# Performance work log

Measured on AMD Instinct MI355X. Metric: run time of the kernel, lower is better.

The kernel has to match this reference:

```python
import jax, jax.numpy as jnp
import numpy as np

B, N, C = 16, 4096, 64          # batch, input points, feature channels
NPOINT, NSAMPLE = 1024, 32      # FPS centroids, neighbors per group
MLP = [64, 64, 128]


def setup_inputs() -> dict:
    key = jax.random.key(0)
    ks = jax.random.split(key, 8)
    xyz = jax.random.uniform(ks[0], (B, N, 3), jnp.float32)
    points = jax.random.normal(ks[1], (B, N, C), jnp.float32)
    inp = {"xyz": xyz, "points": points}
    dims = [3 + C] + MLP  # use_xyz=True -> concat local coords
    for i in range(3):
        inp[f"w{i}"] = jax.random.normal(ks[2 + i], (dims[i], dims[i + 1]), jnp.float32) * (1.0 / np.sqrt(dims[i]))
        inp[f"b{i}"] = jnp.zeros((dims[i + 1],), jnp.float32)
    return inp


def _fps(pts, npoint):
    # iterative farthest point sampling for one cloud (N,3) -> (npoint,) int32
    n = pts.shape[0]
    def step(carry, _):
        dists, last = carry
        d = jnp.sum((pts - pts[last]) ** 2, axis=-1)
        dists = jnp.minimum(dists, d)
        return (dists, jnp.argmax(dists).astype(jnp.int32)), last
    _, idx = jax.lax.scan(step, (jnp.full((n,), 1e10, pts.dtype), jnp.int32(0)), None, length=npoint)
    return idx


def _knn(new_xyz, xyz, k):
    # squared distances (B,S,N) -> k nearest indices (B,S,k)
    d = (jnp.sum(new_xyz ** 2, -1)[..., None]
         - 2.0 * jnp.einsum('bsd,bnd->bsn', new_xyz, xyz)
         + jnp.sum(xyz ** 2, -1)[:, None, :])
    _, idx = jax.lax.top_k(-d, k)
    return idx


def reference(xyz, points, w0, b0, w1, b1, w2, b2):
    bidx = jnp.arange(B)[:, None, None]
    fps_idx = jax.vmap(lambda p: _fps(p, NPOINT))(xyz)            # (B,S)
    new_xyz = jnp.take_along_axis(xyz, fps_idx[..., None], axis=1)  # (B,S,3)
    idx = _knn(new_xyz, xyz, NSAMPLE)                             # (B,S,K)
    grouped_xyz = xyz[bidx, idx] - new_xyz[:, :, None, :]         # local coords (B,S,K,3)
    grouped_pts = points[bidx, idx]                               # (B,S,K,C)
    new_points = jnp.concatenate([grouped_xyz, grouped_pts], axis=-1)
    for w, bias in ((w0, b0), (w1, b1), (w2, b2)):                # 1x1 conv2d MLP
        new_points = jax.nn.relu(jnp.einsum('bskc,cf->bskf', new_points, w) + bias)
    new_points = jnp.max(new_points, axis=2)                      # max over neighbors
    return new_xyz, new_points
```

## Files before the change

kernel.cpp:

```cpp
#include <hip/hip_runtime.h>

#define NB 16
#define NPTS 4096
#define NC 64
#define NS 1024
#define NK 32

typedef float v2f __attribute__((ext_vector_type(2)));
typedef short bf16x8 __attribute__((ext_vector_type(8)));
typedef float f32x4 __attribute__((ext_vector_type(4)));

#define DPP_ROR_I(x, N) __builtin_amdgcn_update_dpp(0, (int)(x), 0x120 + (N), 0xf, 0xf, false)
#define MFMA16(a, b, c) __builtin_amdgcn_mfma_f32_16x16x32_bf16((a), (b), (c), 0, 0, 0)

static __device__ __forceinline__ float max3f(float a, float b, float c) {
    return fmaxf(fmaxf(a, b), c);
}
static __device__ __forceinline__ unsigned min3u(unsigned a, unsigned b, unsigned c) {
    const unsigned m = a < b ? a : b;
    return m < c ? m : c;
}
static __device__ __forceinline__ unsigned short f2bf(float f) {
    const unsigned u = __float_as_uint(f);
    const unsigned r = 0x7FFFu + ((u >> 16) & 1u);
    return (unsigned short)((u + r) >> 16);
}
static __device__ __forceinline__ float bf2f(unsigned short h) {
    return __uint_as_float(((unsigned)h) << 16);
}
static __device__ __forceinline__ unsigned pkhi(float a, float b) {
    return (unsigned)f2bf(a) | ((unsigned)f2bf(b) << 16);
}
static __device__ __forceinline__ unsigned pklo(float a, float b) {
    const float la = a - bf2f(f2bf(a));
    const float lb = b - bf2f(f2bf(b));
    return (unsigned)f2bf(la) | ((unsigned)f2bf(lb) << 16);
}

__global__ __launch_bounds__(256) void fps_kernel(const float* __restrict__ xyz,
                                                  float* __restrict__ out_xyz) {
    __shared__ float4 pts4[NPTS];
    __shared__ float hx[NS], hy[NS], hz[NS];
    __shared__ unsigned wk[2][4][2];

    const int b = blockIdx.x;
    const int t = threadIdx.x;
    const int wv = t >> 6;
    const int lane = t & 63;

    const float* xb = xyz + (size_t)b * NPTS * 3;
    for (int i = t; i < NPTS; i += 256) {
        pts4[i] = make_float4(xb[3 * i], xb[3 * i + 1], xb[3 * i + 2], 0.0f);
    }
    __syncthreads();

    v2f PX[8], PY[8], PZ[8];
    float dm[16];
#pragma unroll
    for (int k = 0; k < 8; ++k) {
        const float4 p0 = pts4[t + (2 * k) * 256];
        const float4 p1 = pts4[t + (2 * k + 1) * 256];
        PX[k].x = p0.x; PX[k].y = p1.x;
        PY[k].x = p0.y; PY[k].y = p1.y;
        PZ[k].x = p0.z; PZ[k].y = p1.z;
        dm[2 * k] = 1e10f; dm[2 * k + 1] = 1e10f;
    }

    const float4 c0 = pts4[0];
    float cx = c0.x, cy = c0.y, cz = c0.z;

    for (int s = 0; s < NS; ++s) {
        if (t == 0) { hx[s] = cx; hy[s] = cy; hz[s] = cz; }

        const v2f cX = { cx, cx };
        const v2f cY = { cy, cy };
        const v2f cZ = { cz, cz };
#pragma unroll
        for (int k = 0; k < 8; ++k) {
            const v2f dX = PX[k] - cX;
            const v2f dY = PY[k] - cY;
            const v2f dZ = PZ[k] - cZ;
            const v2f t1 = dX * dX;
            const v2f t2 = dY * dY;
            const v2f t3 = dZ * dZ;
            const v2f ss = (t1 + t2) + t3;
            dm[2 * k] = fminf(dm[2 * k], ss.x);
            dm[2 * k + 1] = fminf(dm[2 * k + 1], ss.y);
        }

        const float ta = max3f(dm[0], dm[1], dm[2]);
        const float tb = max3f(dm[3], dm[4], dm[5]);
        const float tc = max3f(dm[6], dm[7], dm[8]);
        const float td = max3f(dm[9], dm[10], dm[11]);
        const float te = max3f(dm[12], dm[13], dm[14]);
        const float mv = fmaxf(max3f(ta, tb, tc), max3f(td, te, dm[15]));

        unsigned u[16];
#pragma unroll
        for (int j = 0; j < 16; ++j)
            u[j] = (dm[j] == mv) ? (unsigned)(t + j * 256) : 0xFFFFFFFFu;
        const unsigned ua = min3u(u[0], u[1], u[2]);
        const unsigned ub = min3u(u[3], u[4], u[5]);
        const unsigned uc = min3u(u[6], u[7], u[8]);
        const unsigned ud = min3u(u[9], u[10], u[11]);
        const unsigned ue = min3u(u[12], u[13], u[14]);
        const unsigned uf = min3u(ua, ub, uc);
        const unsigned ug = min3u(ud, ue, u[15]);
        const unsigned best = uf < ug ? uf : ug;

        float r = mv;
        { const float o = __int_as_float(DPP_ROR_I(__float_as_int(r), 1)); r = fmaxf(r, o); }
        { const float o = __int_as_float(DPP_ROR_I(__float_as_int(r), 2)); r = fmaxf(r, o); }
        { const float o = __int_as_float(DPP_ROR_I(__float_as_int(r), 4)); r = fmaxf(r, o); }
        { const float o = __int_as_float(DPP_ROR_I(__float_as_int(r), 8)); r = fmaxf(r, o); }
        const float q0 = __int_as_float(__builtin_amdgcn_readlane(__float_as_int(r), 0));
        const float q1 = __int_as_float(__builtin_amdgcn_readlane(__float_as_int(r), 16));
        const float q2 = __int_as_float(__builtin_amdgcn_readlane(__float_as_int(r), 32));
        const float q3 = __int_as_float(__builtin_amdgcn_readlane(__float_as_int(r), 48));
        const float wm = fmaxf(fmaxf(q0, q1), fmaxf(q2, q3));

        unsigned c = (mv == wm) ? best : 0xFFFFFFFFu;
        { const unsigned o = (unsigned)DPP_ROR_I(c, 1); c = o < c ? o : c; }
        { const unsigned o = (unsigned)DPP_ROR_I(c, 2); c = o < c ? o : c; }
        { const unsigned o = (unsigned)DPP_ROR_I(c, 4); c = o < c ? o : c; }
        { const unsigned o = (unsigned)DPP_ROR_I(c, 8); c = o < c ? o : c; }
        const unsigned g0 = (unsigned)__builtin_amdgcn_readlane((int)c, 0);
        const unsigned g1 = (unsigned)__builtin_amdgcn_readlane((int)c, 16);
        const unsigned g2 = (unsigned)__builtin_amdgcn_readlane((int)c, 32);
        const unsigned g3 = (unsigned)__builtin_amdgcn_readlane((int)c, 48);
        const unsigned ga = g0 < g1 ? g0 : g1;
        const unsigned gb = g2 < g3 ? g2 : g3;
        const unsigned wgi = ga < gb ? ga : gb;

        if (lane == 0) { wk[s & 1][wv][0] = __float_as_uint(wm); wk[s & 1][wv][1] = ~wgi; }
        __syncthreads();
        const unsigned long long k0 = ((unsigned long long)wk[s & 1][0][0] << 32) | wk[s & 1][0][1];
        const unsigned long long k1 = ((unsigned long long)wk[s & 1][1][0] << 32) | wk[s & 1][1][1];
        const unsigned long long k2 = ((unsigned long long)wk[s & 1][2][0] << 32) | wk[s & 1][2][1];
        const unsigned long long k3 = ((unsigned long long)wk[s & 1][3][0] << 32) | wk[s & 1][3][1];
        const unsigned long long ka = k0 > k1 ? k0 : k1;
        const unsigned long long kb = k2 > k3 ? k2 : k3;
        const unsigned long long kw = ka > kb ? ka : kb;

        const int wi = (int)(~(unsigned)kw);
        const float4 cc = pts4[wi];
        cx = cc.x; cy = cc.y; cz = cc.z;
    }

    __syncthreads();
    float* ob = out_xyz + (size_t)b * NS * 3;
#pragma unroll
    for (int r2 = 0; r2 < 12; ++r2) {
        const int f = t + r2 * 256;
        const int i = f / 3;
        const int cmp = f - 3 * i;
        const float v = (cmp == 0) ? hx[i] : ((cmp == 1) ? hy[i] : hz[i]);
        ob[f] = v;
    }
}

#define KNN_INF 3.0e38f

__global__ __launch_bounds__(1024) void knn_kernel(const float* __restrict__ xyz,
                                                   const float* __restrict__ newxyz,
                                                   unsigned short* __restrict__ knn) {
    __shared__ float4 pts[NPTS];

    const int b = blockIdx.x >> 6;
    const int t = threadIdx.x;
    const float* xb = xyz + (size_t)b * NPTS * 3;
    for (int i = t; i < NPTS; i += 1024) {
        const float x = xb[3 * i], y = xb[3 * i + 1], z = xb[3 * i + 2];
        const float ps = __fadd_rn(__fadd_rn(__fmul_rn(x, x), __fmul_rn(y, y)), __fmul_rn(z, z));
        pts[i] = make_float4(x, y, z, ps);
    }
    __syncthreads();

    const int lane = t & 63;
    const int wv = t >> 6;
    const int s = ((blockIdx.x & 63) << 4) + wv;

    const float* q = newxyz + ((size_t)b * NS + s) * 3;
    const float qx = q[0], qy = q[1], qz = q[2];
    const float qs = __fadd_rn(__fadd_rn(__fmul_rn(qx, qx), __fmul_rn(qy, qy)), __fmul_rn(qz, qz));

    float v0 = KNN_INF, v1 = KNN_INF, v2 = KNN_INF, v3 = KNN_INF;
    int i0 = 0, i1 = 0, i2 = 0, i3 = 0;
    unsigned long long rem = 0ull;

#pragma unroll 4
    for (int j = 0; j < 64; ++j) {
        const float4 p = pts[j * 64 + lane];
        const float dot = __fmaf_rn(qz, p.z, __fmaf_rn(qy, p.y, __fmul_rn(qx, p.x)));
        const float d = __fadd_rn(__fsub_rn(qs, __fadd_rn(dot, dot)), p.w);
        const int gi = j * 64 + lane;
        const bool c0 = d < v0, c1 = d < v1, c2 = d < v2, c3 = d < v3;
        v3 = c3 ? (c2 ? v2 : d) : v3;  i3 = c3 ? (c2 ? i2 : gi) : i3;
        v2 = c2 ? (c1 ? v1 : d) : v2;  i2 = c2 ? (c1 ? i1 : gi) : i2;
        v1 = c1 ? (c0 ? v0 : d) : v1;  i1 = c1 ? (c0 ? i0 : gi) : i1;
        v0 = c0 ? d : v0;              i0 = c0 ? gi : i0;
    }

    int kidx = 0;
#pragma unroll 1
    for (int r = 0; r < NK; ++r) {
        float rv = v0;
        { const float o = __int_as_float(DPP_ROR_I(__float_as_int(rv), 1)); rv = fminf(rv, o); }
        { const float o = __int_as_float(DPP_ROR_I(__float_as_int(rv), 2)); rv = fminf(rv, o); }
        { const float o = __int_as_float(DPP_ROR_I(__float_as_int(rv), 4)); rv = fminf(rv, o); }
        { const float o = __int_as_float(DPP_ROR_I(__float_as_int(rv), 8)); rv = fminf(rv, o); }
        const float q0v = __int_as_float(__builtin_amdgcn_readlane(__float_as_int(rv), 0));
        const float q1v = __int_as_float(__builtin_amdgcn_readlane(__float_as_int(rv), 16));
        const float q2v = __int_as_float(__builtin_amdgcn_readlane(__float_as_int(rv), 32));
        const float q3v = __int_as_float(__builtin_amdgcn_readlane(__float_as_int(rv), 48));
        const float wm = fminf(fminf(q0v, q1v), fminf(q2v, q3v));

        unsigned cand = (v0 == wm) ? (unsigned)i0 : 0x7FFFFFFFu;
        { const unsigned o = (unsigned)DPP_ROR_I(cand, 1); cand = o < cand ? o : cand; }
        { const unsigned o = (unsigned)DPP_ROR_I(cand, 2); cand = o < cand ? o : cand; }
        { const unsigned o = (unsigned)DPP_ROR_I(cand, 4); cand = o < cand ? o : cand; }
        { const unsigned o = (unsigned)DPP_ROR_I(cand, 8); cand = o < cand ? o : cand; }
        const unsigned c0r = (unsigned)__builtin_amdgcn_readlane((int)cand, 0);
        const unsigned c1r = (unsigned)__builtin_amdgcn_readlane((int)cand, 16);
        const unsigned c2r = (unsigned)__builtin_amdgcn_readlane((int)cand, 32);
        const unsigned c3r = (unsigned)__builtin_amdgcn_readlane((int)cand, 48);
        const unsigned ca = c0r < c1r ? c0r : c1r;
        const unsigned cb = c2r < c3r ? c2r : c3r;
        const int bi = (int)(ca < cb ? ca : cb);

        if (lane == r) kidx = bi;
        if ((bi & 63) == lane) {
            v0 = v1; i0 = i1;
            v1 = v2; i1 = i2;
            v2 = v3; i2 = i3;
            v3 = KNN_INF;
            rem |= 1ull << (bi >> 6);
            if (v0 >= 1e37f) {
                v0 = v1 = v2 = v3 = KNN_INF;
#pragma unroll 1
                for (int j = 0; j < 64; ++j) {
                    if (!((rem >> j) & 1ull)) {
                        const float4 p = pts[j * 64 + lane];
                        const float dot = __fmaf_rn(qz, p.z, __fmaf_rn(qy, p.y, __fmul_rn(qx, p.x)));
                        const float d = __fadd_rn(__fsub_rn(qs, __fadd_rn(dot, dot)), p.w);
                        const int gi = j * 64 + lane;
                        const bool c0 = d < v0, c1 = d < v1, c2 = d < v2, c3 = d < v3;
                        v3 = c3 ? (c2 ? v2 : d) : v3;  i3 = c3 ? (c2 ? i2 : gi) : i3;
                        v2 = c2 ? (c1 ? v1 : d) : v2;  i2 = c2 ? (c1 ? i1 : gi) : i2;
                        v1 = c1 ? (c0 ? v0 : d) : v1;  i1 = c1 ? (c0 ? i0 : gi) : i1;
                        v0 = c0 ? d : v0;              i0 = c0 ? gi : i0;
                    }
                }
            }
        }
    }

    if (lane < NK) knn[(((size_t)b * NS + s) << 5) + lane] = (unsigned short)kidx;
}

__global__ __launch_bounds__(256) void mlp_kernel(const float* __restrict__ xyz,
                                                  const float* __restrict__ points,
                                                  const float* __restrict__ newxyz,
                                                  const unsigned short* __restrict__ knn,
                                                  const float* __restrict__ w0, const float* __restrict__ b0,
                                                  const float* __restrict__ w1, const float* __restrict__ b1,
                                                  const float* __restrict__ w2, const float* __restrict__ b2,
                                                  float* __restrict__ out) {
    __shared__ unsigned aHi[64 * 52], aLo[64 * 52];
    __shared__ unsigned bHi[64 * 36], bLo[64 * 36];
    __shared__ int sI[64];

    const int t = threadIdx.x;
    const int lane = t & 63;
    const int wv = t >> 6;
    const int g0 = blockIdx.x * 2;
    const int bb = g0 >> 10;

    if (t < 64) sI[t] = knn[((size_t)g0 + (t >> 5)) * 32 + (t & 31)];
    __syncthreads();

#pragma unroll
    for (int j = 0; j < 4; ++j) {
        const int id = j * 256 + t;
        const int row = id >> 4, qq = id & 15;
        const float4 p = *(const float4*)(points + (((size_t)bb * NPTS + sI[row]) << 6) + qq * 4);
        aHi[row * 52 + qq * 2]     = pkhi(p.x, p.y);
        aHi[row * 52 + qq * 2 + 1] = pkhi(p.z, p.w);
        aLo[row * 52 + qq * 2]     = pklo(p.x, p.y);
        aLo[row * 52 + qq * 2 + 1] = pklo(p.z, p.w);
    }
    if (t < 64) {
        const int row = t;
        const int idx = sI[row];
        const int gg = g0 + (row >> 5);
        const float* pp = xyz + ((size_t)bb * NPTS + idx) * 3;
        const float* qn = newxyz + (size_t)gg * 3;
        const float dx = pp[0] - qn[0];
        const float dy = pp[1] - qn[1];
        const float dz = pp[2] - qn[2];
        aHi[row * 52 + 32] = pkhi(dx, dy);
        aHi[row * 52 + 33] = pkhi(dz, 0.0f);
        aLo[row * 52 + 32] = pklo(dx, dy);
        aLo[row * 52 + 33] = pklo(dz, 0.0f);
    }
#pragma unroll
    for (int j = 0; j < 4; ++j) {
        const int id = j * 256 + t;
        const int row = id >> 4, c = 34 + (id & 15);
        aHi[row * 52 + c] = 0u;
        aLo[row * 52 + c] = 0u;
    }

    const int col0 = (wv << 4) + (lane & 15);
    const int kb = (lane >> 4) << 3;
    bf16x8 w0h[3], w0l[3];
#pragma unroll
    for (int kt = 0; kt < 3; ++kt) {
#pragma unroll
        for (int j = 0; j < 8; ++j) {
            const int k = kt * 32 + kb + j;
            const int worig = (k < 64) ? (k + 3) : ((k < 67) ? (k - 64) : -1);
            const float v = (worig >= 0) ? w0[worig * 64 + col0] : 0.0f;
            const unsigned short h = f2bf(v);
            w0h[kt][j] = (short)h;
            w0l[kt][j] = (short)f2bf(v - bf2f(h));
        }
    }
    const float bias0 = b0[col0];
    __syncthreads();

#pragma unroll
    for (int mt = 0; mt < 4; ++mt) {
        f32x4 acc = { bias0, bias0, bias0, bias0 };
#pragma unroll
        for (int kt = 0; kt < 3; ++kt) {
            const int base = (mt * 16 + (lane & 15)) * 52 + kt * 16 + ((lane >> 4) << 2);
            const bf16x8 ah = *(const bf16x8*)&aHi[base];
            const bf16x8 al = *(const bf16x8*)&aLo[base];
            acc = MFMA16(ah, w0h[kt], acc);
            acc = MFMA16(al, w0h[kt], acc);
            acc = MFMA16(ah, w0l[kt], acc);
        }
#pragma unroll
        for (int r = 0; r < 4; ++r) {
            const float v = fmaxf(acc[r], 0.0f);
            const int row = mt * 16 + ((lane >> 4) << 2) + r;
            const unsigned short h = f2bf(v);
            ((unsigned short*)bHi)[row * 72 + col0] = h;
            ((unsigned short*)bLo)[row * 72 + col0] = f2bf(v - bf2f(h));
        }
    }

    bf16x8 w1h[2], w1l[2];
#pragma unroll
    for (int kt = 0; kt < 2; ++kt) {
#pragma unroll
        for (int j = 0; j < 8; ++j) {
            const int k = kt * 32 + kb + j;
            const float v = w1[k * 64 + col0];
            const unsigned short h = f2bf(v);
            w1h[kt][j] = (short)h;
            w1l[kt][j] = (short)f2bf(v - bf2f(h));
        }
    }
    const float bias1 = b1[col0];
    __syncthreads();

#pragma unroll
    for (int mt = 0; mt < 4; ++mt) {
        f32x4 acc = { bias1, bias1, bias1, bias1 };
#pragma unroll
        for (int kt = 0; kt < 2; ++kt) {
            const int base = (mt * 16 + (lane & 15)) * 36 + kt * 16 + ((lane >> 4) << 2);
            const bf16x8 ah = *(const bf16x8*)&bHi[base];
            const bf16x8 al = *(const bf16x8*)&bLo[base];
            acc = MFMA16(ah, w1h[kt], acc);
            acc = MFMA16(al, w1h[kt], acc);
            acc = MFMA16(ah, w1l[kt], acc);
        }
#pragma unroll
        for (int r = 0; r < 4; ++r) {
            const float v = fmaxf(acc[r], 0.0f);
            const int row = mt * 16 + ((lane >> 4) << 2) + r;
            const unsigned short h = f2bf(v);
            ((unsigned short*)aHi)[row * 72 + col0] = h;
            ((unsigned short*)aLo)[row * 72 + col0] = f2bf(v - bf2f(h));
        }
    }

    const int colB = ((wv + 4) << 4) + (lane & 15);
    bf16x8 w2ha[2], w2la[2], w2hb[2], w2lb[2];
#pragma unroll
    for (int kt = 0; kt < 2; ++kt) {
#pragma unroll
        for (int j = 0; j < 8; ++j) {
            const int k = kt * 32 + kb + j;
            float v = w2[k * 128 + col0];
            unsigned short h = f2bf(v);
            w2ha[kt][j] = (short)h;
            w2la[kt][j] = (short)f2bf(v - bf2f(h));
            v = w2[k * 128 + colB];
            h = f2bf(v);
            w2hb[kt][j] = (short)h;
            w2lb[kt][j] = (short)f2bf(v - bf2f(h));
        }
    }
    const float bias2a = b2[col0];
    const float bias2b = b2[colB];
    __syncthreads();

#pragma unroll
    for (int gj = 0; gj < 2; ++gj) {
        f32x4 aA[2], aB[2];
#pragma unroll
        for (int hh = 0; hh < 2; ++hh) {
            const int mt = gj * 2 + hh;
            f32x4 accA = { bias2a, bias2a, bias2a, bias2a };
            f32x4 accB = { bias2b, bias2b, bias2b, bias2b };
#pragma unroll
            for (int kt = 0; kt < 2; ++kt) {
                const int base = (mt * 16 + (lane & 15)) * 36 + kt * 16 + ((lane >> 4) << 2);
                const bf16x8 ah = *(const bf16x8*)&aHi[base];
                const bf16x8 al = *(const bf16x8*)&aLo[base];
                accA = MFMA16(ah, w2ha[kt], accA);
                accA = MFMA16(al, w2ha[kt], accA);
                accA = MFMA16(ah, w2la[kt], accA);
                accB = MFMA16(ah, w2hb[kt], accB);
                accB = MFMA16(al, w2hb[kt], accB);
                accB = MFMA16(ah, w2lb[kt], accB);
            }
            aA[hh] = accA;
            aB[hh] = accB;
        }
        float mA = max3f(max3f(aA[0][0], aA[0][1], aA[0][2]),
                         max3f(aA[0][3], aA[1][0], aA[1][1]),
                         fmaxf(aA[1][2], aA[1][3]));
        float mB = max3f(max3f(aB[0][0], aB[0][1], aB[0][2]),
                         max3f(aB[0][3], aB[1][0], aB[1][1]),
                         fmaxf(aB[1][2], aB[1][3]));
        mA = fmaxf(mA, __shfl_xor(mA, 16));
        mA = fmaxf(mA, __shfl_xor(mA, 32));
        mB = fmaxf(mB, __shfl_xor(mB, 16));
        mB = fmaxf(mB, __shfl_xor(mB, 32));
        mA = fmaxf(mA, 0.0f);
        mB = fmaxf(mB, 0.0f);
        float* op = out + (size_t)(g0 + gj) * 128;
        if (lane < 16) {
            op[(wv << 4) + lane] = mA;
            op[((wv + 4) << 4) + lane] = mB;
        }
    }
}

extern "C" void kernel_launch(void* const* d_in, const int* in_sizes, int n_in,
                              void* d_out, int out_size, void* d_ws, size_t ws_size,
                              hipStream_t stream) {
    const float* xyz    = (const float*)d_in[0];
    const float* points = (const float*)d_in[1];
    const float* w0 = (const float*)d_in[2];
    const float* b0 = (const float*)d_in[3];
    const float* w1 = (const float*)d_in[4];
    const float* b1 = (const float*)d_in[5];
    const float* w2 = (const float*)d_in[6];
    const float* b2 = (const float*)d_in[7];

    float* out = (float*)d_out;
    float* newxyz = out;
    float* newpts = out + (size_t)NB * NS * 3;
    unsigned short* knn = (unsigned short*)d_ws;

    fps_kernel<<<NB, 256, 0, stream>>>(xyz, newxyz);
    knn_kernel<<<NB * (NS / 16), 1024, 0, stream>>>(xyz, newxyz, knn);
    mlp_kernel<<<(NB * NS) / 2, 256, 0, stream>>>(xyz, points, newxyz, knn,
                                                  w0, b0, w1, b1, w2, b2, newpts);
}
```

Before: 820.9 us.

## Fuse FPS, kNN and MLP into one persistent kernel with progress flags

Replaces the three launches with a single persistent kernel of 256 blocks. The first 16 blocks run farthest point sampling and publish progress counters in workspace memory, while the remaining blocks run kNN and the MLP on centroid chunks as they become ready. The aim is to overlap the long serial FPS phase with downstream work and to drop the intermediate kNN round trip through global memory. It relies on all blocks being co-resident, adds spin-wait synchronisation, and cuts kNN/MLP parallelism to a fixed block count.

```diff
diff --git a/kernel.cpp b/kernel.cpp
--- a/kernel.cpp
+++ b/kernel.cpp
@@ -37,417 +37,431 @@
     return (unsigned)f2bf(la) | ((unsigned)f2bf(lb) << 16);
 }
 
-__global__ __launch_bounds__(256) void fps_kernel(const float* __restrict__ xyz,
-                                                  float* __restrict__ out_xyz) {
-    __shared__ float4 pts4[NPTS];
-    __shared__ float hx[NS], hy[NS], hz[NS];
-    __shared__ unsigned wk[2][4][2];
-
-    const int b = blockIdx.x;
-    const int t = threadIdx.x;
-    const int wv = t >> 6;
-    const int lane = t & 63;
-
-    const float* xb = xyz + (size_t)b * NPTS * 3;
-    for (int i = t; i < NPTS; i += 256) {
-        pts4[i] = make_float4(xb[3 * i], xb[3 * i + 1], xb[3 * i + 2], 0.0f);
-    }
-    __syncthreads();
-
-    v2f PX[8], PY[8], PZ[8];
-    float dm[16];
-#pragma unroll
-    for (int k = 0; k < 8; ++k) {
-        const float4 p0 = pts4[t + (2 * k) * 256];
-        const float4 p1 = pts4[t + (2 * k + 1) * 256];
-        PX[k].x = p0.x; PX[k].y = p1.x;
-        PY[k].x = p0.y; PY[k].y = p1.y;
-        PZ[k].x = p0.z; PZ[k].y = p1.z;
-        dm[2 * k] = 1e10f; dm[2 * k + 1] = 1e10f;
-    }
-
-    const float4 c0 = pts4[0];
-    float cx = c0.x, cy = c0.y, cz = c0.z;
-
-    for (int s = 0; s < NS; ++s) {
-        if (t == 0) { hx[s] = cx; hy[s] = cy; hz[s] = cz; }
-
-        const v2f cX = { cx, cx };
-        const v2f cY = { cy, cy };
-        const v2f cZ = { cz, cz };
-#pragma unroll
-        for (int k = 0; k < 8; ++k) {
-            const v2f dX = PX[k] - cX;
-            const v2f dY = PY[k] - cY;
-            const v2f dZ = PZ[k] - cZ;
-            const v2f t1 = dX * dX;
-            const v2f t2 = dY * dY;
-            const v2f t3 = dZ * dZ;
-            const v2f ss = (t1 + t2) + t3;
-            dm[2 * k] = fminf(dm[2 * k], ss.x);
-            dm[2 * k + 1] = fminf(dm[2 * k + 1], ss.y);
-        }
-
-        const float ta = max3f(dm[0], dm[1], dm[2]);
-        const float tb = max3f(dm[3], dm[4], dm[5]);
-        const float tc = max3f(dm[6], dm[7], dm[8]);
-        const float td = max3f(dm[9], dm[10], dm[11]);
-        const float te = max3f(dm[12], dm[13], dm[14]);
-        const float mv = fmaxf(max3f(ta, tb, tc), max3f(td, te, dm[15]));
-
-        unsigned u[16];
-#pragma unroll
-        for (int j = 0; j < 16; ++j)
-            u[j] = (dm[j] == mv) ? (unsigned)(t + j * 256) : 0xFFFFFFFFu;
-        const unsigned ua = min3u(u[0], u[1], u[2]);
-        const unsigned ub = min3u(u[3], u[4], u[5]);
-        const unsigned uc = min3u(u[6], u[7], u[8]);
-        const unsigned ud = min3u(u[9], u[10], u[11]);
-        const unsigned ue = min3u(u[12], u[13], u[14]);
-        const unsigned uf = min3u(ua, ub, uc);
-        const unsigned ug = min3u(ud, ue, u[15]);
-        const unsigned best = uf < ug ? uf : ug;
-
-        float r = mv;
-        { const float o = __int_as_float(DPP_ROR_I(__float_as_int(r), 1)); r = fmaxf(r, o); }
-        { const float o = __int_as_float(DPP_ROR_I(__float_as_int(r), 2)); r = fmaxf(r, o); }
-        { const float o = __int_as_float(DPP_ROR_I(__float_as_int(r), 4)); r = fmaxf(r, o); }
-        { const float o = __int_as_float(DPP_ROR_I(__float_as_int(r), 8)); r = fmaxf(r, o); }
-        const float q0 = __int_as_float(__builtin_amdgcn_readlane(__float_as_int(r), 0));
-        const float q1 = __int_as_float(__builtin_amdgcn_readlane(__float_as_int(r), 16));
-        const float q2 = __int_as_float(__builtin_amdgcn_readlane(__float_as_int(r), 32));
-        const float q3 = __int_as_float(__builtin_amdgcn_readlane(__float_as_int(r), 48));
-        const float wm = fmaxf(fmaxf(q0, q1), fmaxf(q2, q3));
-
-        unsigned c = (mv == wm) ? best : 0xFFFFFFFFu;
-        { const unsigned o = (unsigned)DPP_ROR_I(c, 1); c = o < c ? o : c; }
-        { const unsigned o = (unsigned)DPP_ROR_I(c, 2); c = o < c ? o : c; }
-        { const unsigned o = (unsigned)DPP_ROR_I(c, 4); c = o < c ? o : c; }
-        { const unsigned o = (unsigned)DPP_ROR_I(c, 8); c = o < c ? o : c; }
-        const unsigned g0 = (unsigned)__builtin_amdgcn_readlane((int)c, 0);
-        const unsigned g1 = (unsigned)__builtin_amdgcn_readlane((int)c, 16);
-        const unsigned g2 = (unsigned)__builtin_amdgcn_readlane((int)c, 32);
-        const unsigned g3 = (unsigned)__builtin_amdgcn_readlane((int)c, 48);
-        const unsigned ga = g0 < g1 ? g0 : g1;
-        const unsigned gb = g2 < g3 ? g2 : g3;
-        const unsigned wgi = ga < gb ? ga : gb;
-
-        if (lane == 0) { wk[s & 1][wv][0] = __float_as_uint(wm); wk[s & 1][wv][1] = ~wgi; }
-        __syncthreads();
-        const unsigned long long k0 = ((unsigned long long)wk[s & 1][0][0] << 32) | wk[s & 1][0][1];
-        const unsigned long long k1 = ((unsigned long long)wk[s & 1][1][0] << 32) | wk[s & 1][1][1];
-        const unsigned long long k2 = ((unsigned long long)wk[s & 1][2][0] << 32) | wk[s & 1][2][1];
-        const unsigned long long k3 = ((unsigned long long)wk[s & 1][3][0] << 32) | wk[s & 1][3][1];
-        const unsigned long long ka = k0 > k1 ? k0 : k1;
-        const unsigned long long kb = k2 > k3 ? k2 : k3;
-        const unsigned long long kw = ka > kb ? ka : kb;
-
-        const int wi = (int)(~(unsigned)kw);
-        const float4 cc = pts4[wi];
-        cx = cc.x; cy = cc.y; cz = cc.z;
-    }
-
-    __syncthreads();
-    float* ob = out_xyz + (size_t)b * NS * 3;
-#pragma unroll
-    for (int r2 = 0; r2 < 12; ++r2) {
-        const int f = t + r2 * 256;
-        const int i = f / 3;
-        const int cmp = f - 3 * i;
-        const float v = (cmp == 0) ? hx[i] : ((cmp == 1) ? hy[i] : hz[i]);
-        ob[f] = v;
-    }
-}
-
 #define KNN_INF 3.0e38f
 
-__global__ __launch_bounds__(1024) void knn_kernel(const float* __restrict__ xyz,
-                                                   const float* __restrict__ newxyz,
-                                                   unsigned short* __restrict__ knn) {
-    __shared__ float4 pts[NPTS];
-
-    const int b = blockIdx.x >> 6;
-    const int t = threadIdx.x;
-    const float* xb = xyz + (size_t)b * NPTS * 3;
-    for (int i = t; i < NPTS; i += 1024) {
-        const float x = xb[3 * i], y = xb[3 * i + 1], z = xb[3 * i + 2];
-        const float ps = __fadd_rn(__fadd_rn(__fmul_rn(x, x), __fmul_rn(y, y)), __fmul_rn(z, z));
-        pts[i] = make_float4(x, y, z, ps);
-    }
-    __syncthreads();
-
-    const int lane = t & 63;
-    const int wv = t >> 6;
-    const int s = ((blockIdx.x & 63) << 4) + wv;
-
-    const float* q = newxyz + ((size_t)b * NS + s) * 3;
-    const float qx = q[0], qy = q[1], qz = q[2];
-    const float qs = __fadd_rn(__fadd_rn(__fmul_rn(qx, qx), __fmul_rn(qy, qy)), __fmul_rn(qz, qz));
-
-    float v0 = KNN_INF, v1 = KNN_INF, v2 = KNN_INF, v3 = KNN_INF;
-    int i0 = 0, i1 = 0, i2 = 0, i3 = 0;
-    unsigned long long rem = 0ull;
-
-#pragma unroll 4
-    for (int j = 0; j < 64; ++j) {
-        const float4 p = pts[j * 64 + lane];
-        const float dot = __fmaf_rn(qz, p.z, __fmaf_rn(qy, p.y, __fmul_rn(qx, p.x)));
-        const float d = __fadd_rn(__fsub_rn(qs, __fadd_rn(dot, dot)), p.w);
-        const int gi = j * 64 + lane;
-        const bool c0 = d < v0, c1 = d < v1, c2 = d < v2, c3 = d < v3;
-        v3 = c3 ? (c2 ? v2 : d) : v3;  i3 = c3 ? (c2 ? i2 : gi) : i3;
-        v2 = c2 ? (c1 ? v1 : d) : v2;  i2 = c2 ? (c1 ? i1 : gi) : i2;
-        v1 = c1 ? (c0 ? v0 : d) : v1;  i1 = c1 ? (c0 ? i0 : gi) : i1;
-        v0 = c0 ? d : v0;              i0 = c0 ? gi : i0;
-    }
-
-    int kidx = 0;
-#pragma unroll 1
-    for (int r = 0; r < NK; ++r) {
-        float rv = v0;
-        { const float o = __int_as_float(DPP_ROR_I(__float_as_int(rv), 1)); rv = fminf(rv, o); }
-        { const float o = __int_as_float(DPP_ROR_I(__float_as_int(rv), 2)); rv = fminf(rv, o); }
-        { const float o = __int_as_float(DPP_ROR_I(__float_as_int(rv), 4)); rv = fminf(rv, o); }
-        { const float o = __int_as_float(DPP_ROR_I(__float_as_int(rv), 8)); rv = fminf(rv, o); }
-        const float q0v = __int_as_float(__builtin_amdgcn_readlane(__float_as_int(rv), 0));
-        const float q1v = __int_as_float(__builtin_amdgcn_readlane(__float_as_int(rv), 16));
-        const float q2v = __int_as_float(__builtin_amdgcn_readlane(__float_as_int(rv), 32));
-        const float q3v = __int_as_float(__builtin_amdgcn_readlane(__float_as_int(rv), 48));
-        const float wm = fminf(fminf(q0v, q1v), fminf(q2v, q3v));
-
-        unsigned cand = (v0 == wm) ? (unsigned)i0 : 0x7FFFFFFFu;
-        { const unsigned o = (unsigned)DPP_ROR_I(cand, 1); cand = o < cand ? o : cand; }
-        { const unsigned o = (unsigned)DPP_ROR_I(cand, 2); cand = o < cand ? o : cand; }
-        { const unsigned o = (unsigned)DPP_ROR_I(cand, 4); cand = o < cand ? o : cand; }
-        { const unsigned o = (unsigned)DPP_ROR_I(cand, 8); cand = o < cand ? o : cand; }
-        const unsigned c0r = (unsigned)__builtin_amdgcn_readlane((int)cand, 0);
-        const unsigned c1r = (unsigned)__builtin_amdgcn_readlane((int)cand, 16);
-        const unsigned c2r = (unsigned)__builtin_amdgcn_readlane((int)cand, 32);
-        const unsigned c3r = (unsigned)__builtin_amdgcn_readlane((int)cand, 48);
-        const unsigned ca = c0r < c1r ? c0r : c1r;
-        const unsigned cb = c2r < c3r ? c2r : c3r;
-        const int bi = (int)(ca < cb ? ca : cb);
-
-        if (lane == r) kidx = bi;
-        if ((bi & 63) == lane) {
-            v0 = v1; i0 = i1;
-            v1 = v2; i1 = i2;
-            v2 = v3; i2 = i3;
-            v3 = KNN_INF;
-            rem |= 1ull << (bi >> 6);
-            if (v0 >= 1e37f) {
-                v0 = v1 = v2 = v3 = KNN_INF;
-#pragma unroll 1
-                for (int j = 0; j < 64; ++j) {
-                    if (!((rem >> j) & 1ull)) {
-                        const float4 p = pts[j * 64 + lane];
-                        const float dot = __fmaf_rn(qz, p.z, __fmaf_rn(qy, p.y, __fmul_rn(qx, p.x)));
-                        const float d = __fadd_rn(__fsub_rn(qs, __fadd_rn(dot, dot)), p.w);
-                        const int gi = j * 64 + lane;
-                        const bool c0 = d < v0, c1 = d < v1, c2 = d < v2, c3 = d < v3;
-                        v3 = c3 ? (c2 ? v2 : d) : v3;  i3 = c3 ? (c2 ? i2 : gi) : i3;
-                        v2 = c2 ? (c1 ? v1 : d) : v2;  i2 = c2 ? (c1 ? i1 : gi) : i2;
-                        v1 = c1 ? (c0 ? v0 : d) : v1;  i1 = c1 ? (c0 ? i0 : gi) : i1;
-                        v0 = c0 ? d : v0;              i0 = c0 ? gi : i0;
-                    }
-                }
-            }
-        }
-    }
-
-    if (lane < NK) knn[(((size_t)b * NS + s) << 5) + lane] = (unsigned short)kidx;
-}
-
-__global__ __launch_bounds__(256) void mlp_kernel(const float* __restrict__ xyz,
-                                                  const float* __restrict__ points,
-                                                  const float* __restrict__ newxyz,
-                                                  const unsigned short* __restrict__ knn,
-                                                  const float* __restrict__ w0, const float* __restrict__ b0,
-                                                  const float* __restrict__ w1, const float* __restrict__ b1,
-                                                  const float* __restrict__ w2, const float* __restrict__ b2,
-                                                  float* __restrict__ out) {
-    __shared__ unsigned aHi[64 * 52], aLo[64 * 52];
-    __shared__ unsigned bHi[64 * 36], bLo[64 * 36];
-    __shared__ int sI[64];
+#define SMEM_BYTES 111168
+
+__global__ __launch_bounds__(256) void fused_kernel(
+        const float* __restrict__ xyz, const float* __restrict__ points,
+        const float* __restrict__ w0, const float* __restrict__ b0,
+        const float* __restrict__ w1, const float* __restrict__ b1,
+        const float* __restrict__ w2, const float* __restrict__ b2,
+        float* __restrict__ out, unsigned* __restrict__ progress) {
+    __shared__ __align__(16) char smem[SMEM_BYTES];
+    float4* pts = (float4*)smem;
 
     const int t = threadIdx.x;
     const int lane = t & 63;
     const int wv = t >> 6;
-    const int g0 = blockIdx.x * 2;
-    const int bb = g0 >> 10;
-
-    if (t < 64) sI[t] = knn[((size_t)g0 + (t >> 5)) * 32 + (t & 31)];
-    __syncthreads();
-
-#pragma unroll
-    for (int j = 0; j < 4; ++j) {
-        const int id = j * 256 + t;
-        const int row = id >> 4, qq = id & 15;
-        const float4 p = *(const float4*)(points + (((size_t)bb * NPTS + sI[row]) << 6) + qq * 4);
-        aHi[row * 52 + qq * 2]     = pkhi(p.x, p.y);
-        aHi[row * 52 + qq * 2 + 1] = pkhi(p.z, p.w);
-        aLo[row * 52 + qq * 2]     = pklo(p.x, p.y);
-        aLo[row * 52 + qq * 2 + 1] = pklo(p.z, p.w);
-    }
-    if (t < 64) {
-        const int row = t;
-        const int idx = sI[row];
-        const int gg = g0 + (row >> 5);
-        const float* pp = xyz + ((size_t)bb * NPTS + idx) * 3;
-        const float* qn = newxyz + (size_t)gg * 3;
-        const float dx = pp[0] - qn[0];
-        const float dy = pp[1] - qn[1];
-        const float dz = pp[2] - qn[2];
-        aHi[row * 52 + 32] = pkhi(dx, dy);
-        aHi[row * 52 + 33] = pkhi(dz, 0.0f);
-        aLo[row * 52 + 32] = pklo(dx, dy);
-        aLo[row * 52 + 33] = pklo(dz, 0.0f);
-    }
-#pragma unroll
-    for (int j = 0; j < 4; ++j) {
-        const int id = j * 256 + t;
-        const int row = id >> 4, c = 34 + (id & 15);
-        aHi[row * 52 + c] = 0u;
-        aLo[row * 52 + c] = 0u;
-    }
-
-    const int col0 = (wv << 4) + (lane & 15);
-    const int kb = (lane >> 4) << 3;
-    bf16x8 w0h[3], w0l[3];
-#pragma unroll
-    for (int kt = 0; kt < 3; ++kt) {
-#pragma unroll
-        for (int j = 0; j < 8; ++j) {
-            const int k = kt * 32 + kb + j;
-            const int worig = (k < 64) ? (k + 3) : ((k < 67) ? (k - 64) : -1);
-            const float v = (worig >= 0) ? w0[worig * 64 + col0] : 0.0f;
-            const unsigned short h = f2bf(v);
-            w0h[kt][j] = (short)h;
-            w0l[kt][j] = (short)f2bf(v - bf2f(h));
+    float* newxyz = out;
+    float* outpts = out + (size_t)NB * NS * 3;
+
+    if (blockIdx.x < NB) {
+        float* hist = (float*)(smem + 65536);
+        unsigned* wk = (unsigned*)(smem + 65536 + 12288);
+        const int b = blockIdx.x;
+
+        const float* xb = xyz + (size_t)b * NPTS * 3;
+        for (int i = t; i < NPTS; i += 256) {
+            pts[i] = make_float4(xb[3 * i], xb[3 * i + 1], xb[3 * i + 2], 0.0f);
         }
-    }
-    const float bias0 = b0[col0];
-    __syncthreads();
-
-#pragma unroll
-    for (int mt = 0; mt < 4; ++mt) {
-        f32x4 acc = { bias0, bias0, bias0, bias0 };
-#pragma unroll
-        for (int kt = 0; kt < 3; ++kt) {
-            const int base = (mt * 16 + (lane & 15)) * 52 + kt * 16 + ((lane >> 4) << 2);
-            const bf16x8 ah = *(const bf16x8*)&aHi[base];
-            const bf16x8 al = *(const bf16x8*)&aLo[base];
-            acc = MFMA16(ah, w0h[kt], acc);
-            acc = MFMA16(al, w0h[kt], acc);
-            acc = MFMA16(ah, w0l[kt], acc);
+        __syncthreads();
+
+        v2f PX[8], PY[8], PZ[8];
+        float dm[16];
+#pragma unroll
+        for (int k = 0; k < 8; ++k) {
+            const float4 p0 = pts[t + (2 * k) * 256];
+            const float4 p1 = pts[t + (2 * k + 1) * 256];
+            PX[k].x = p0.x; PX[k].y = p1.x;
+            PY[k].x = p0.y; PY[k].y = p1.y;
+            PZ[k].x = p0.z; PZ[k].y = p1.z;
+            dm[2 * k] = 1e10f; dm[2 * k + 1] = 1e10f;
         }
-#pragma unroll
-        for (int r = 0; r < 4; ++r) {
-            const float v = fmaxf(acc[r], 0.0f);
-            const int row = mt * 16 + ((lane >> 4) << 2) + r;
-            const unsigned short h = f2bf(v);
-            ((unsigned short*)bHi)[row * 72 + col0] = h;
-            ((unsigned short*)bLo)[row * 72 + col0] = f2bf(v - bf2f(h));
+
+        const float4 c0 = pts[0];
+        float cx = c0.x, cy = c0.y, cz = c0.z;
+        float* ob = newxyz + (size_t)b * NS * 3;
+
+        for (int s = 0; s < NS; ++s) {
+            if (t == 0) { hist[s] = cx; hist[1024 + s] = cy; hist[2048 + s] = cz; }
+
+            const v2f cX = { cx, cx };
+            const v2f cY = { cy, cy };
+            const v2f cZ = { cz, cz };
+#pragma unroll
+            for (int k = 0; k < 8; ++k) {
+                const v2f dX = PX[k] - cX;
+                const v2f dY = PY[k] - cY;
+                const v2f dZ = PZ[k] - cZ;
+                const v2f t1 = dX * dX;
+                const v2f t2 = dY * dY;
+                const v2f t3 = dZ * dZ;
+                const v2f ss = (t1 + t2) + t3;
+                dm[2 * k] = fminf(dm[2 * k], ss.x);
+                dm[2 * k + 1] = fminf(dm[2 * k + 1], ss.y);
+            }
+
+            const float ta = max3f(dm[0], dm[1], dm[2]);
+            const float tb = max3f(dm[3], dm[4], dm[5]);
+            const float tc = max3f(dm[6], dm[7], dm[8]);
+            const float td = max3f(dm[9], dm[10], dm[11]);
+            const float te = max3f(dm[12], dm[13], dm[14]);
+            const float mv = fmaxf(max3f(ta, tb, tc), max3f(td, te, dm[15]));
+
+            unsigned u[16];
+#pragma unroll
+            for (int j = 0; j < 16; ++j)
+                u[j] = (dm[j] == mv) ? (unsigned)(t + j * 256) : 0xFFFFFFFFu;
+            const unsigned ua = min3u(u[0], u[1], u[2]);
+            const unsigned ub = min3u(u[3], u[4], u[5]);
+            const unsigned uc = min3u(u[6], u[7], u[8]);
+            const unsigned ud = min3u(u[9], u[10], u[11]);
+            const unsigned ue = min3u(u[12], u[13], u[14]);
+            const unsigned uf = min3u(ua, ub, uc);
+            const unsigned ug = min3u(ud, ue, u[15]);
+            const unsigned best = uf < ug ? uf : ug;
+
+            float r = mv;
+            { const float o = __int_as_float(DPP_ROR_I(__float_as_int(r), 1)); r = fmaxf(r, o); }
+            { const float o = __int_as_float(DPP_ROR_I(__float_as_int(r), 2)); r = fmaxf(r, o); }
+            { const float o = __int_as_float(DPP_ROR_I(__float_as_int(r), 4)); r = fmaxf(r, o); }
+            { const float o = __int_as_float(DPP_ROR_I(__float_as_int(r), 8)); r = fmaxf(r, o); }
+            const float q0 = __int_as_float(__builtin_amdgcn_readlane(__float_as_int(r), 0));
+            const float q1 = __int_as_float(__builtin_amdgcn_readlane(__float_as_int(r), 16));
+            const float q2 = __int_as_float(__builtin_amdgcn_readlane(__float_as_int(r), 32));
+            const float q3 = __int_as_float(__builtin_amdgcn_readlane(__float_as_int(r), 48));
+            const float wm = fmaxf(fmaxf(q0, q1), fmaxf(q2, q3));
+
+            unsigned c = (mv == wm) ? best : 0xFFFFFFFFu;
+            { const unsigned o = (unsigned)DPP_ROR_I(c, 1); c = o < c ? o : c; }
+            { const unsigned o = (unsigned)DPP_ROR_I(c, 2); c = o < c ? o : c; }
+            { const unsigned o = (unsigned)DPP_ROR_I(c, 4); c = o < c ? o : c; }
+            { const unsigned o = (unsigned)DPP_ROR_I(c, 8); c = o < c ? o : c; }
+            const unsigned g0v = (unsigned)__builtin_amdgcn_readlane((int)c, 0);
+            const unsigned g1v = (unsigned)__builtin_amdgcn_readlane((int)c, 16);
+            const unsigned g2v = (unsigned)__builtin_amdgcn_readlane((int)c, 32);
+            const unsigned g3v = (unsigned)__builtin_amdgcn_readlane((int)c, 48);
+            const unsigned ga = g0v < g1v ? g0v : g1v;
+            const unsigned gb = g2v < g3v ? g2v : g3v;
+            const unsigned wgi = ga < gb ? ga : gb;
+
+            if (lane == 0) { wk[((s & 1) * 4 + wv) * 2] = __float_as_uint(wm); wk[((s & 1) * 4 + wv) * 2 + 1] = ~wgi; }
+            __syncthreads();
+            const unsigned* wb = &wk[(s & 1) * 8];
+            const unsigned long long k0 = ((unsigned long long)wb[0] << 32) | wb[1];
+            const unsigned long long k1 = ((unsigned long long)wb[2] << 32) | wb[3];
+            const unsigned long long k2 = ((unsigned long long)wb[4] << 32) | wb[5];
+            const unsigned long long k3 = ((unsigned long long)wb[6] << 32) | wb[7];
+            const unsigned long long ka = k0 > k1 ? k0 : k1;
+            const unsigned long long kb = k2 > k3 ? k2 : k3;
+            const unsigned long long kw = ka > kb ? ka : kb;
+
+            if ((s & 15) == 15) {
+                if (t < 64) {
+                    if (t < 48) {
+                        const int f = (s & ~15) * 3 + t;
+                        ob[f] = hist[(f % 3) * 1024 + f / 3];
+                    }
+                    __threadfence();
+                }
+                if (t == 0)
+                    __hip_atomic_fetch_add(&progress[b], 16u, __ATOMIC_RELEASE, __HIP_MEMORY_SCOPE_AGENT);
+            }
+
+            const int wi = (int)(~(unsigned)kw);
+            const float4 cc = pts[wi];
+            cx = cc.x; cy = cc.y; cz = cc.z;
         }
-    }
-
-    bf16x8 w1h[2], w1l[2];
-#pragma unroll
-    for (int kt = 0; kt < 2; ++kt) {
-#pragma unroll
-        for (int j = 0; j < 8; ++j) {
-            const int k = kt * 32 + kb + j;
-            const float v = w1[k * 64 + col0];
-            const unsigned short h = f2bf(v);
-            w1h[kt][j] = (short)h;
-            w1l[kt][j] = (short)f2bf(v - bf2f(h));
+    } else {
+        unsigned* aHi = (unsigned*)(smem + 65536);
+        unsigned* aLo = aHi + 64 * 52;
+        unsigned* bHi = aLo + 64 * 52;
+        unsigned* bLo = bHi + 64 * 36;
+        int* sIc = (int*)(bLo + 64 * 36);
+        float* nqc = (float*)(sIc + 128);
+
+        const int w = blockIdx.x - NB;
+        const int batch = w & 15;
+        const int widx = w >> 4;
+
+        const float* xb = xyz + (size_t)batch * NPTS * 3;
+        for (int i = t; i < NPTS; i += 256) {
+            const float x = xb[3 * i], y = xb[3 * i + 1], z = xb[3 * i + 2];
+            const float ps = __fadd_rn(__fadd_rn(__fmul_rn(x, x), __fmul_rn(y, y)), __fmul_rn(z, z));
+            pts[i] = make_float4(x, y, z, ps);
         }
-    }
-    const float bias1 = b1[col0];
-    __syncthreads();
-
-#pragma unroll
-    for (int mt = 0; mt < 4; ++mt) {
-        f32x4 acc = { bias1, bias1, bias1, bias1 };
-#pragma unroll
-        for (int kt = 0; kt < 2; ++kt) {
-            const int base = (mt * 16 + (lane & 15)) * 36 + kt * 16 + ((lane >> 4) << 2);
-            const bf16x8 ah = *(const bf16x8*)&bHi[base];
-            const bf16x8 al = *(const bf16x8*)&bLo[base];
-            acc = MFMA16(ah, w1h[kt], acc);
-            acc = MFMA16(al, w1h[kt], acc);
-            acc = MFMA16(ah, w1l[kt], acc);
-        }
-#pragma unroll
-        for (int r = 0; r < 4; ++r) {
-            const float v = fmaxf(acc[r], 0.0f);
-            const int row = mt * 16 + ((lane >> 4) << 2) + r;
-            const unsigned short h = f2bf(v);
-            ((unsigned short*)aHi)[row * 72 + col0] = h;
-            ((unsigned short*)aLo)[row * 72 + col0] = f2bf(v - bf2f(h));
-        }
-    }
-
-    const int colB = ((wv + 4) << 4) + (lane & 15);
-    bf16x8 w2ha[2], w2la[2], w2hb[2], w2lb[2];
-#pragma unroll
-    for (int kt = 0; kt < 2; ++kt) {
-#pragma unroll
-        for (int j = 0; j < 8; ++j) {
-            const int k = kt * 32 + kb + j;
-            float v = w2[k * 128 + col0];
-            unsigned short h = f2bf(v);
-            w2ha[kt][j] = (short)h;
-            w2la[kt][j] = (short)f2bf(v - bf2f(h));
-            v = w2[k * 128 + colB];
-            h = f2bf(v);
-            w2hb[kt][j] = (short)h;
-            w2lb[kt][j] = (short)f2bf(v - bf2f(h));
-        }
-    }
-    const float bias2a = b2[col0];
-    const float bias2b = b2[colB];
-    __syncthreads();
-
-#pragma unroll
-    for (int gj = 0; gj < 2; ++gj) {
-        f32x4 aA[2], aB[2];
-#pragma unroll
-        for (int hh = 0; hh < 2; ++hh) {
-            const int mt = gj * 2 + hh;
-            f32x4 accA = { bias2a, bias2a, bias2a, bias2a };
-            f32x4 accB = { bias2b, bias2b, bias2b, bias2b };
-#pragma unroll
-            for (int kt = 0; kt < 2; ++kt) {
-                const int base = (mt * 16 + (lane & 15)) * 36 + kt * 16 + ((lane >> 4) << 2);
-                const bf16x8 ah = *(const bf16x8*)&aHi[base];
-                const bf16x8 al = *(const bf16x8*)&aLo[base];
-                accA = MFMA16(ah, w2ha[kt], accA);
-                accA = MFMA16(al, w2ha[kt], accA);
-                accA = MFMA16(ah, w2la[kt], accA);
-                accB = MFMA16(ah, w2hb[kt], accB);
-                accB = MFMA16(al, w2hb[kt], accB);
-                accB = MFMA16(ah, w2lb[kt], accB);
+        __syncthreads();
+
+        const int col0 = (wv << 4) + (lane & 15);
+        const int kb = (lane >> 4) << 3;
+
+        for (int chunk = widx; chunk < 256; chunk += 15) {
+            const int s0 = chunk * 4;
+            if (t == 0) {
+                while (__hip_atomic_load(&progress[batch], __ATOMIC_ACQUIRE, __HIP_MEMORY_SCOPE_AGENT)
+                       < (unsigned)(s0 + 4))
+                    __builtin_amdgcn_s_sleep(16);
             }
-            aA[hh] = accA;
-            aB[hh] = accB;
-        }
-        float mA = max3f(max3f(aA[0][0], aA[0][1], aA[0][2]),
-                         max3f(aA[0][3], aA[1][0], aA[1][1]),
-                         fmaxf(aA[1][2], aA[1][3]));
-        float mB = max3f(max3f(aB[0][0], aB[0][1], aB[0][2]),
-                         max3f(aB[0][3], aB[1][0], aB[1][1]),
-                         fmaxf(aB[1][2], aB[1][3]));
-        mA = fmaxf(mA, __shfl_xor(mA, 16));
-        mA = fmaxf(mA, __shfl_xor(mA, 32));
-        mB = fmaxf(mB, __shfl_xor(mB, 16));
-        mB = fmaxf(mB, __shfl_xor(mB, 32));
-        mA = fmaxf(mA, 0.0f);
-        mB = fmaxf(mB, 0.0f);
-        float* op = out + (size_t)(g0 + gj) * 128;
-        if (lane < 16) {
-            op[(wv << 4) + lane] = mA;
-            op[((wv + 4) << 4) + lane] = mB;
+            __syncthreads();
+
+            {
+                const int s = s0 + wv;
+                const unsigned* qp = (const unsigned*)(newxyz + ((size_t)batch * NS + s) * 3);
+                const float qx = __uint_as_float(__hip_atomic_load(qp + 0, __ATOMIC_RELAXED, __HIP_MEMORY_SCOPE_AGENT));
+                const float qy = __uint_as_float(__hip_atomic_load(qp + 1, __ATOMIC_RELAXED, __HIP_MEMORY_SCOPE_AGENT));
+                const float qz = __uint_as_float(__hip_atomic_load(qp + 2, __ATOMIC_RELAXED, __HIP_MEMORY_SCOPE_AGENT));
+                const float qs = __fadd_rn(__fadd_rn(__fmul_rn(qx, qx), __fmul_rn(qy, qy)), __fmul_rn(qz, qz));
+
+                float v0 = KNN_INF, v1 = KNN_INF, v2 = KNN_INF, v3 = KNN_INF;
+                int i0 = 0, i1 = 0, i2 = 0, i3 = 0;
+                unsigned long long rem = 0ull;
+
+#pragma unroll 4
+                for (int j = 0; j < 64; ++j) {
+                    const float4 p = pts[j * 64 + lane];
+                    const float dot = __fmaf_rn(qz, p.z, __fmaf_rn(qy, p.y, __fmul_rn(qx, p.x)));
+                    const float d = __fadd_rn(__fsub_rn(qs, __fadd_rn(dot, dot)), p.w);
+                    const int gi = j * 64 + lane;
+                    const bool c0 = d < v0, c1 = d < v1, c2 = d < v2, c3 = d < v3;
+                    v3 = c3 ? (c2 ? v2 : d) : v3;  i3 = c3 ? (c2 ? i2 : gi) : i3;
+                    v2 = c2 ? (c1 ? v1 : d) : v2;  i2 = c2 ? (c1 ? i1 : gi) : i2;
+                    v1 = c1 ? (c0 ? v0 : d) : v1;  i1 = c1 ? (c0 ? i0 : gi) : i1;
+                    v0 = c0 ? d : v0;              i0 = c0 ? gi : i0;
+                }
+
+                int kidx = 0;
+#pragma unroll 1
+                for (int r = 0; r < NK; ++r) {
+                    float rv = v0;
+                    { const float o = __int_as_float(DPP_ROR_I(__float_as_int(rv), 1)); rv = fminf(rv, o); }
+                    { const float o = __int_as_float(DPP_ROR_I(__float_as_int(rv), 2)); rv = fminf(rv, o); }
+                    { const float o = __int_as_float(DPP_ROR_I(__float_as_int(rv), 4)); rv = fminf(rv, o); }
+                    { const float o = __int_as_float(DPP_ROR_I(__float_as_int(rv), 8)); rv = fminf(rv, o); }
+                    const float q0v = __int_as_float(__builtin_amdgcn_readlane(__float_as_int(rv), 0));
+                    const float q1v = __int_as_float(__builtin_amdgcn_readlane(__float_as_int(rv), 16));
+                    const float q2v = __int_as_float(__builtin_amdgcn_readlane(__float_as_int(rv), 32));
+                    const float q3v = __int_as_float(__builtin_amdgcn_readlane(__float_as_int(rv), 48));
+                    const float wm = fminf(fminf(q0v, q1v), fminf(q2v, q3v));
+
+                    unsigned cand = (v0 == wm) ? (unsigned)i0 : 0x7FFFFFFFu;
+                    { const unsigned o = (unsigned)DPP_ROR_I(cand, 1); cand = o < cand ? o : cand; }
+                    { const unsigned o = (unsigned)DPP_ROR_I(cand, 2); cand = o < cand ? o : cand; }
+                    { const unsigned o = (unsigned)DPP_ROR_I(cand, 4); cand = o < cand ? o : cand; }
+                    { const unsigned o = (unsigned)DPP_ROR_I(cand, 8); cand = o < cand ? o : cand; }
+                    const unsigned c0r = (unsigned)__builtin_amdgcn_readlane((int)cand, 0);
+                    const unsigned c1r = (unsigned)__builtin_amdgcn_readlane((int)cand, 16);
+                    const unsigned c2r = (unsigned)__builtin_amdgcn_readlane((int)cand, 32);
+                    const unsigned c3r = (unsigned)__builtin_amdgcn_readlane((int)cand, 48);
+                    const unsigned ca = c0r < c1r ? c0r : c1r;
+                    const unsigned cb = c2r < c3r ? c2r : c3r;
+                    const int bi = (int)(ca < cb ? ca : cb);
+
+                    if (lane == r) kidx = bi;
+                    if ((bi & 63) == lane) {
+                        v0 = v1; i0 = i1;
+                        v1 = v2; i1 = i2;
+                        v2 = v3; i2 = i3;
+                        v3 = KNN_INF;
+                        rem |= 1ull << (bi >> 6);
+                        if (v0 >= 1e37f) {
+                            v0 = v1 = v2 = v3 = KNN_INF;
+#pragma unroll 1
+                            for (int j = 0; j < 64; ++j) {
+                                if (!((rem >> j) & 1ull)) {
+                                    const float4 p = pts[j * 64 + lane];
+                                    const float dot = __fmaf_rn(qz, p.z, __fmaf_rn(qy, p.y, __fmul_rn(qx, p.x)));
+                                    const float d = __fadd_rn(__fsub_rn(qs, __fadd_rn(dot, dot)), p.w);
+                                    const int gi = j * 64 + lane;
+                                    const bool c0 = d < v0, c1 = d < v1, c2 = d < v2, c3 = d < v3;
+                                    v3 = c3 ? (c2 ? v2 : d) : v3;  i3 = c3 ? (c2 ? i2 : gi) : i3;
+                                    v2 = c2 ? (c1 ? v1 : d) : v2;  i2 = c2 ? (c1 ? i1 : gi) : i2;
+                                    v1 = c1 ? (c0 ? v0 : d) : v1;  i1 = c1 ? (c0 ? i0 : gi) : i1;
+                                    v0 = c0 ? d : v0;              i0 = c0 ? gi : i0;
+                                }
+                            }
+                        }
+                    }
+                }
+
+                if (lane < NK) sIc[wv * 32 + lane] = kidx;
+                if (lane == 0) { nqc[wv * 3] = qx; nqc[wv * 3 + 1] = qy; nqc[wv * 3 + 2] = qz; }
+            }
+
+#pragma unroll 1
+            for (int uu = 0; uu < 2; ++uu) {
+                __syncthreads();
+
+#pragma unroll
+                for (int j = 0; j < 4; ++j) {
+                    const int id = j * 256 + t;
+                    const int row = id >> 4, qq = id & 15;
+                    const int idx = sIc[uu * 64 + row];
+                    const float4 p = *(const float4*)(points + (((size_t)batch * NPTS + idx) << 6) + qq * 4);
+                    aHi[row * 52 + qq * 2]     = pkhi(p.x, p.y);
+                    aHi[row * 52 + qq * 2 + 1] = pkhi(p.z, p.w);
+                    aLo[row * 52 + qq * 2]     = pklo(p.x, p.y);
+                    aLo[row * 52 + qq * 2 + 1] = pklo(p.z, p.w);
+                }
+                if (t < 64) {
+                    const int row = t;
+                    const int idx = sIc[uu * 64 + row];
+                    const int lq = 2 * uu + (row >> 5);
+                    const float* pp = xyz + ((size_t)batch * NPTS + idx) * 3;
+                    const float dx = pp[0] - nqc[lq * 3];
+                    const float dy = pp[1] - nqc[lq * 3 + 1];
+                    const float dz = pp[2] - nqc[lq * 3 + 2];
+                    aHi[row * 52 + 32] = pkhi(dx, dy);
+                    aHi[row * 52 + 33] = pkhi(dz, 0.0f);
+                    aLo[row * 52 + 32] = pklo(dx, dy);
+                    aLo[row * 52 + 33] = pklo(dz, 0.0f);
+                }
+#pragma unroll
+                for (int j = 0; j < 4; ++j) {
+                    const int id = j * 256 + t;
+                    const int row = id >> 4, c = 34 + (id & 15);
+                    aHi[row * 52 + c] = 0u;
+                    aLo[row * 52 + c] = 0u;
+                }
+
+                bf16x8 w0h[3], w0l[3];
+#pragma unroll
+                for (int kt = 0; kt < 3; ++kt) {
+#pragma unroll
+                    for (int j = 0; j < 8; ++j) {
+                        const int k = kt * 32 + kb + j;
+                        const int worig = (k < 64) ? (k + 3) : ((k < 67) ? (k - 64) : -1);
+                        const float v = (worig >= 0) ? w0[worig * 64 + col0] : 0.0f;
+                        const unsigned short h = f2bf(v);
+                        w0h[kt][j] = (short)h;
+                        w0l[kt][j] = (short)f2bf(v - bf2f(h));
+                    }
+                }
+                const float bias0 = b0[col0];
+                __syncthreads();
+
+#pragma unroll
+                for (int mt = 0; mt < 4; ++mt) {
+                    f32x4 acc = { bias0, bias0, bias0, bias0 };
+#pragma unroll
+                    for (int kt = 0; kt < 3; ++kt) {
+                        const int base = (mt * 16 + (lane & 15)) * 52 + kt * 16 + ((lane >> 4) << 2);
+                        const bf16x8 ah = *(const bf16x8*)&aHi[base];
+                        const bf16x8 al = *(const bf16x8*)&aLo[base];
+                        acc = MFMA16(ah, w0h[kt], acc);
+                        acc = MFMA16(al, w0h[kt], acc);
+                        acc = MFMA16(ah, w0l[kt], acc);
+                    }
+#pragma unroll
+                    for (int r = 0; r < 4; ++r) {
+                        const float v = fmaxf(acc[r], 0.0f);
+                        const int row = mt * 16 + ((lane >> 4) << 2) + r;
+                        const unsigned short h = f2bf(v);
+                        ((unsigned short*)bHi)[row * 72 + col0] = h;
+                        ((unsigned short*)bLo)[row * 72 + col0] = f2bf(v - bf2f(h));
+                    }
+                }
+
+                bf16x8 w1h[2], w1l[2];
+#pragma unroll
+                for (int kt = 0; kt < 2; ++kt) {
+#pragma unroll
+                    for (int j = 0; j < 8; ++j) {
+                        const int k = kt * 32 + kb + j;
+                        const float v = w1[k * 64 + col0];
+                        const unsigned short h = f2bf(v);
+                        w1h[kt][j] = (short)h;
+                        w1l[kt][j] = (short)f2bf(v - bf2f(h));
+                    }
+                }
+                const float bias1 = b1[col0];
+                __syncthreads();
+
+#pragma unroll
+                for (int mt = 0; mt < 4; ++mt) {
+                    f32x4 acc = { bias1, bias1, bias1, bias1 };
+#pragma unroll
+                    for (int kt = 0; kt < 2; ++kt) {
+                        const int base = (mt * 16 + (lane & 15)) * 36 + kt * 16 + ((lane >> 4) << 2);
+                        const bf16x8 ah = *(const bf16x8*)&bHi[base];
+                        const bf16x8 al = *(const bf16x8*)&bLo[base];
+                        acc = MFMA16(ah, w1h[kt], acc);
+                        acc = MFMA16(al, w1h[kt], acc);
+                        acc = MFMA16(ah, w1l[kt], acc);
+                    }
+#pragma unroll
+                    for (int r = 0; r < 4; ++r) {
+                        const float v = fmaxf(acc[r], 0.0f);
+                        const int row = mt * 16 + ((lane >> 4) << 2) + r;
+                        const unsigned short h = f2bf(v);
+                        ((unsigned short*)aHi)[row * 72 + col0] = h;
+                        ((unsigned short*)aLo)[row * 72 + col0] = f2bf(v - bf2f(h));
+                    }
+                }
+
+                const int colB = ((wv + 4) << 4) + (lane & 15);
+                bf16x8 w2ha[2], w2la[2], w2hb[2], w2lb[2];
+#pragma unroll
+                for (int kt = 0; kt < 2; ++kt) {
+#pragma unroll
+                    for (int j = 0; j < 8; ++j) {
+                        const int k = kt * 32 + kb + j;
+                        float v = w2[k * 128 + col0];
+                        unsigned short h = f2bf(v);
+                        w2ha[kt][j] = (short)h;
+                        w2la[kt][j] = (short)f2bf(v - bf2f(h));
+                        v = w2[k * 128 + colB];
+                        h = f2bf(v);
+                        w2hb[kt][j] = (short)h;
+                        w2lb[kt][j] = (short)f2bf(v - bf2f(h));
+                    }
+                }
+                const float bias2a = b2[col0];
+                const float bias2b = b2[colB];
+                __syncthreads();
+
+#pragma unroll
+                for (int gj = 0; gj < 2; ++gj) {
+                    f32x4 aA[2], aB[2];
+#pragma unroll
+                    for (int hh = 0; hh < 2; ++hh) {
+                        const int mt = gj * 2 + hh;
+                        f32x4 accA = { bias2a, bias2a, bias2a, bias2a };
+                        f32x4 accB = { bias2b, bias2b, bias2b, bias2b };
+#pragma unroll
+                        for (int kt = 0; kt < 2; ++kt) {
+                            const int base = (mt * 16 + (lane & 15)) * 36 + kt * 16 + ((lane >> 4) << 2);
+                            const bf16x8 ah = *(const bf16x8*)&aHi[base];
+                            const bf16x8 al = *(const bf16x8*)&aLo[base];
+                            accA = MFMA16(ah, w2ha[kt], accA);
+                            accA = MFMA16(al, w2ha[kt], accA);
+                            accA = MFMA16(ah, w2la[kt], accA);
+                            accB = MFMA16(ah, w2hb[kt], accB);
+                            accB = MFMA16(al, w2hb[kt], accB);
+                            accB = MFMA16(ah, w2lb[kt], accB);
+                        }
+                        aA[hh] = accA;
+                        aB[hh] = accB;
+                    }
+                    float mA = max3f(max3f(aA[0][0], aA[0][1], aA[0][2]),
+                                     max3f(aA[0][3], aA[1][0], aA[1][1]),
+                                     fmaxf(aA[1][2], aA[1][3]));
+                    float mB = max3f(max3f(aB[0][0], aB[0][1], aB[0][2]),
+                                     max3f(aB[0][3], aB[1][0], aB[1][1]),
+                                     fmaxf(aB[1][2], aB[1][3]));
+                    mA = fmaxf(mA, __shfl_xor(mA, 16));
+                    mA = fmaxf(mA, __shfl_xor(mA, 32));
+                    mB = fmaxf(mB, __shfl_xor(mB, 16));
+                    mB = fmaxf(mB, __shfl_xor(mB, 32));
+                    mA = fmaxf(mA, 0.0f);
+                    mB = fmaxf(mB, 0.0f);
+                    float* op = outpts + (size_t)((size_t)batch * NS + s0 + 2 * uu + gj) * 128;
+                    if (lane < 16) {
+                        op[(wv << 4) + lane] = mA;
+                        op[((wv + 4) << 4) + lane] = mB;
+                    }
+                }
+            }
         }
     }
 }
@@ -464,13 +478,9 @@
     const float* w2 = (const float*)d_in[6];
     const float* b2 = (const float*)d_in[7];
 
-    float* out = (float*)d_out;
-    float* newxyz = out;
-    float* newpts = out + (size_t)NB * NS * 3;
-    unsigned short* knn = (unsigned short*)d_ws;
-
-    fps_kernel<<<NB, 256, 0, stream>>>(xyz, newxyz);
-    knn_kernel<<<NB * (NS / 16), 1024, 0, stream>>>(xyz, newxyz, knn);
-    mlp_kernel<<<(NB * NS) / 2, 256, 0, stream>>>(xyz, points, newxyz, knn,
-                                                  w0, b0, w1, b1, w2, b2, newpts);
-}
+    unsigned* progress = (unsigned*)d_ws;
+    hipMemsetAsync(progress, 0, 64, stream);
+
+    fused_kernel<<<256, 256, 0, stream>>>(xyz, points, w0, b0, w1, b1, w2, b2,
+                                          (float*)d_out, progress);
+}
```

New measurement: 739.9 us. 9.9% less time.
